# Kernel optimization log

Hardware: AMD Instinct MI355X
Metric: run time of the kernel (lower is better)

The kernel has to match this reference:

```python
import jax, jax.numpy as jnp
import numpy as np

B, NSV, NTRK, K, H = 512, 128, 512, 8, 16


def setup_inputs() -> dict:
    key = jax.random.key(0)
    ks = jax.random.split(key, 12)
    p = lambda k, shp: (jax.random.normal(k, shp, dtype=jnp.float32) * 0.1)
    return {
        "x_sv": jax.random.normal(ks[0], (B * NSV, 2), dtype=jnp.float32),
        "x_trk": jax.random.normal(ks[1], (B * NTRK, 8), dtype=jnp.float32),
        "batch_sv": jnp.repeat(jnp.arange(B, dtype=jnp.int32), NSV),
        "batch_trk": jnp.repeat(jnp.arange(B, dtype=jnp.int32), NTRK),
        # sv_encode: Linear(2,16) -> ELU -> Linear(16,16)
        "W1s": p(ks[2], (2, H)), "b1s": jnp.zeros((H,), jnp.float32),
        "W2s": p(ks[3], (H, H)), "b2s": jnp.zeros((H,), jnp.float32),
        # trk_encode: Linear(8,16) -> ELU -> Linear(16,16)
        "W1t": p(ks[4], (8, H)), "b1t": jnp.zeros((H,), jnp.float32),
        "W2t": p(ks[5], (H, H)), "b2t": jnp.zeros((H,), jnp.float32),
        # edge MLP: Linear(2*16, 16)
        "We": p(ks[6], (2 * H, H)), "be": jnp.zeros((H,), jnp.float32),
        # output head: Linear(16, 1)
        "Wo": p(ks[7], (H, 1)), "bo": jnp.zeros((1,), jnp.float32),
    }


def reference(x_sv, x_trk, batch_sv, batch_trk,
              W1s, b1s, W2s, b2s, W1t, b1t, W2t, b2t, We, be, Wo, bo):
    # Node encoders
    sv = jax.nn.elu(x_sv @ W1s + b1s) @ W2s + b2s      # [Nsv, H]
    trk = jax.nn.elu(x_trk @ W1t + b1t) @ W2t + b2t    # [Ntrk, H]

    # Regular batching: reshape to per-event blocks (batch_sv/batch_trk are
    # contiguous repeats of arange(B) with NSV / NTRK nodes per event).
    svb = sv.reshape(B, NSV, H)      # [B, S, H]
    trkb = trk.reshape(B, NTRK, H)   # [B, T, H]

    # kNN in encoded space: squared L2 distance per event, k nearest SVs per track
    t_sq = jnp.sum(trkb * trkb, -1)[:, :, None]          # [B, T, 1]
    s_sq = jnp.sum(svb * svb, -1)[:, None, :]            # [B, 1, S]
    dots = jnp.einsum("bth,bsh->bts", trkb, svb)         # [B, T, S]
    d2 = t_sq + s_sq - 2.0 * dots                        # [B, T, S]
    _, idx = jax.lax.top_k(-d2, K)                       # [B, T, K] indices into S

    # Gather neighbor SV features: [B, T, K, H]
    nbr = jax.vmap(lambda s, i: s[i])(svb, idx)

    # EdgeConv message: nn(cat[x_i, x_j - x_i]), x_i = track (target), x_j = SV
    ti = trkb[:, :, None, :]                                    # [B, T, 1, H]
    msg_in = jnp.concatenate(
        [jnp.broadcast_to(ti, nbr.shape), nbr - ti], axis=-1)   # [B, T, K, 2H]
    msg = msg_in @ We + be                                      # [B, T, K, H]
    feats = jnp.max(msg, axis=2).reshape(B * NTRK, H)           # max aggregation

    # Output head + per-event average pool (avg_pool_x with cluster == batch)
    out = jax.nn.sigmoid(feats @ Wo + bo)                       # [Ntrk, 1]
    sums = jax.ops.segment_sum(out, batch_trk, num_segments=B)  # [B, 1]
    cnts = jax.ops.segment_sum(jnp.ones_like(out), batch_trk, num_segments=B)
    pooled = sums / cnts                                        # [B, 1]
    batch_out = jnp.arange(B, dtype=jnp.int32)
    return pooled, batch_out
```

## Files before the change

### kernel.cpp

```cpp
#include <hip/hip_runtime.h>
#include <cmath>

#define BB   512
#define NSV  128
#define NTRK 512
#define KK   8
#define HH   16
#define TPB  512
#define PSTR 20

__device__ __forceinline__ float elu_f(float x) {
    return x > 0.0f ? x : expm1f(x);
}
__device__ __forceinline__ unsigned umin_u(unsigned a, unsigned b) { return a < b ? a : b; }
__device__ __forceinline__ unsigned umax_u(unsigned a, unsigned b) { return a > b ? a : b; }

__global__ __launch_bounds__(TPB, 4) void fused_net(
    const float* __restrict__ x_sv, const float* __restrict__ x_trk,
    const float* __restrict__ W1s, const float* __restrict__ b1s,
    const float* __restrict__ W2s, const float* __restrict__ b2s,
    const float* __restrict__ W1t, const float* __restrict__ b1t,
    const float* __restrict__ W2t, const float* __restrict__ b2t,
    const float* __restrict__ We,  const float* __restrict__ be,
    const float* __restrict__ Wo,  const float* __restrict__ bo,
    float* __restrict__ out)
{
    __shared__ float svf[NSV][HH];
    __shared__ float hsq[NSV];
    __shared__ float proj[NSV][PSTR];
    __shared__ float sWbot[HH][HH];
    __shared__ float sWdiff[HH][HH];
    __shared__ float sW1t[8][HH];
    __shared__ float sW2t[HH][HH];
    __shared__ float sb1t[HH], sb2t[HH], sbe[HH], sWo[HH];
    __shared__ float sred[TPB / 64];
    __shared__ float sbo;

    const int b   = blockIdx.x;
    const int tid = threadIdx.x;

    if (tid < HH * HH) {
        int j = tid >> 4, h = tid & 15;
        float top = We[j * HH + h];
        float bot = We[(HH + j) * HH + h];
        sWbot[j][h]  = bot;
        sWdiff[j][h] = top - bot;
        sW2t[j][h]   = W2t[tid];
    }
    if (tid < 8 * HH) sW1t[tid >> 4][tid & 15] = W1t[tid];
    if (tid < HH) {
        sb1t[tid] = b1t[tid];
        sb2t[tid] = b2t[tid];
        sbe[tid]  = be[tid];
        sWo[tid]  = Wo[tid];
    }
    if (tid == 0) sbo = bo[0];

    if (tid < NSV) {
        const float* xp = x_sv + (size_t)(b * NSV + tid) * 2;
        float x0 = xp[0], x1 = xp[1];
        float hbuf[HH];
        #pragma unroll
        for (int h = 0; h < HH; ++h)
            hbuf[h] = elu_f(x0 * W1s[h] + x1 * W1s[HH + h] + b1s[h]);
        float sq = 0.0f;
        #pragma unroll
        for (int h2 = 0; h2 < HH; ++h2) {
            float a = b2s[h2];
            #pragma unroll
            for (int h = 0; h < HH; ++h) a += hbuf[h] * W2s[h * HH + h2];
            svf[tid][h2] = a;
            sq += a * a;
        }
        hsq[tid] = 0.5f * sq;
    }
    __syncthreads();

    for (int e = tid; e < NSV * HH; e += TPB) {
        int s = e >> 4, h = e & 15;
        float a = 0.0f;
        #pragma unroll
        for (int j = 0; j < HH; ++j) a += svf[s][j] * sWbot[j][h];
        proj[s][h] = a;
    }

    const int t = tid;
    float tf[HH];
    float htsq;
    {
        const float* xp = x_trk + (size_t)(b * NTRK + t) * 8;
        float x[8];
        *(float4*)&x[0] = *(const float4*)&xp[0];
        *(float4*)&x[4] = *(const float4*)&xp[4];
        float hbuf[HH];
        #pragma unroll
        for (int h = 0; h < HH; ++h) {
            float a = sb1t[h];
            #pragma unroll
            for (int i = 0; i < 8; ++i) a += x[i] * sW1t[i][h];
            hbuf[h] = elu_f(a);
        }
        float sq = 0.0f;
        #pragma unroll
        for (int h2 = 0; h2 < HH; ++h2) {
            float a = sb2t[h2];
            #pragma unroll
            for (int h = 0; h < HH; ++h) a += hbuf[h] * sW2t[h][h2];
            tf[h2] = a;
            sq += a * a;
        }
        htsq = 0.5f * sq;
    }

    unsigned k[KK];
    #pragma unroll
    for (int q = 0; q < KK; ++q) k[q] = 0xFFFFFFFFu;
    __syncthreads();

    #pragma unroll 4
    for (int s = 0; s < NSV; ++s) {
        float4 s0 = *(const float4*)&svf[s][0];
        float4 s1 = *(const float4*)&svf[s][4];
        float4 s2 = *(const float4*)&svf[s][8];
        float4 s3 = *(const float4*)&svf[s][12];
        float hs = hsq[s];
        float a0 = fmaf(-tf[0], s0.x, htsq);
        float a1 = fmaf(-tf[1], s0.y, hs);
        float a2 = -tf[2] * s0.z;
        float a3 = -tf[3] * s0.w;
        a0 = fmaf(-tf[4],  s1.x, a0); a1 = fmaf(-tf[5],  s1.y, a1);
        a2 = fmaf(-tf[6],  s1.z, a2); a3 = fmaf(-tf[7],  s1.w, a3);
        a0 = fmaf(-tf[8],  s2.x, a0); a1 = fmaf(-tf[9],  s2.y, a1);
        a2 = fmaf(-tf[10], s2.z, a2); a3 = fmaf(-tf[11], s2.w, a3);
        a0 = fmaf(-tf[12], s3.x, a0); a1 = fmaf(-tf[13], s3.y, a1);
        a2 = fmaf(-tf[14], s3.z, a2); a3 = fmaf(-tf[15], s3.w, a3);
        float e = fmaxf((a0 + a1) + (a2 + a3), 0.0f);
        unsigned v = (__float_as_uint(e) & 0xFFFFFF80u) | (unsigned)s;
        #pragma unroll
        for (int q = 0; q < KK; ++q) {
            unsigned nk = umin_u(v, k[q]);
            v           = umax_u(v, k[q]);
            k[q] = nk;
        }
    }

    float local;
    {
        float base[HH];
        #pragma unroll
        for (int h = 0; h < HH; ++h) {
            float a = sbe[h];
            #pragma unroll
            for (int j = 0; j < HH; ++j) a += tf[j] * sWdiff[j][h];
            base[h] = a;
        }
        float mx[HH];
        #pragma unroll
        for (int h = 0; h < HH; ++h) mx[h] = -INFINITY;
        #pragma unroll
        for (int q = 0; q < KK; ++q) {
            const float* pr = &proj[k[q] & 127u][0];
            #pragma unroll
            for (int h4 = 0; h4 < 4; ++h4) {
                float4 p = *(const float4*)&pr[h4 * 4];
                mx[h4 * 4 + 0] = fmaxf(mx[h4 * 4 + 0], p.x);
                mx[h4 * 4 + 1] = fmaxf(mx[h4 * 4 + 1], p.y);
                mx[h4 * 4 + 2] = fmaxf(mx[h4 * 4 + 2], p.z);
                mx[h4 * 4 + 3] = fmaxf(mx[h4 * 4 + 3], p.w);
            }
        }
        float acc = sbo;
        #pragma unroll
        for (int h = 0; h < HH; ++h) acc += (base[h] + mx[h]) * sWo[h];
        local = 1.0f / (1.0f + expf(-acc));
    }

    #pragma unroll
    for (int off = 32; off > 0; off >>= 1)
        local += __shfl_down(local, off, 64);
    if ((tid & 63) == 0) sred[tid >> 6] = local;
    __syncthreads();
    if (tid == 0) {
        float tot = 0.0f;
        #pragma unroll
        for (int w = 0; w < TPB / 64; ++w) tot += sred[w];
        out[b]      = tot * (1.0f / NTRK);
        out[BB + b] = (float)b;
    }
}

extern "C" void kernel_launch(void* const* d_in, const int* in_sizes, int n_in,
                              void* d_out, int out_size, void* d_ws, size_t ws_size,
                              hipStream_t stream) {
    const float* x_sv  = (const float*)d_in[0];
    const float* x_trk = (const float*)d_in[1];
    const float* W1s = (const float*)d_in[4];
    const float* b1s = (const float*)d_in[5];
    const float* W2s = (const float*)d_in[6];
    const float* b2s = (const float*)d_in[7];
    const float* W1t = (const float*)d_in[8];
    const float* b1t = (const float*)d_in[9];
    const float* W2t = (const float*)d_in[10];
    const float* b2t = (const float*)d_in[11];
    const float* We  = (const float*)d_in[12];
    const float* be  = (const float*)d_in[13];
    const float* Wo  = (const float*)d_in[14];
    const float* bo  = (const float*)d_in[15];
    float* out = (float*)d_out;

    fused_net<<<BB, TPB, 0, stream>>>(x_sv, x_trk,
                                      W1s, b1s, W2s, b2s,
                                      W1t, b1t, W2t, b2t,
                                      We, be, Wo, bo, out);
}
```

Baseline: 136.6 us.

## Split SV encoding into precompute kernel and use med3 top-k insertion

Moves the SV encoder, projection, half-squared norms and weight difference into a separate precompute kernel that writes to workspace. The main kernel then reads SV features straight from global memory (uniform, scalar-cache friendly) instead of LDS, and keeps only proj in LDS. The sorted top-k insertion becomes a v_med3_u32 network, roughly halving the min/max ops per candidate, and weights and biases are read from global instead of staged in shared memory. This costs an extra launch and a global round trip for the SV data.

Result: slower. 139.4 us (+2.0%).

```diff
diff --git a/kernel.cpp b/kernel.cpp
--- a/kernel.cpp
+++ b/kernel.cpp
@@ -13,100 +13,111 @@
     return x > 0.0f ? x : expm1f(x);
 }
 __device__ __forceinline__ unsigned umin_u(unsigned a, unsigned b) { return a < b ? a : b; }
-__device__ __forceinline__ unsigned umax_u(unsigned a, unsigned b) { return a > b ? a : b; }
-
-__global__ __launch_bounds__(TPB, 4) void fused_net(
-    const float* __restrict__ x_sv, const float* __restrict__ x_trk,
+__device__ __forceinline__ unsigned med3u(unsigned a, unsigned b, unsigned c) {
+    unsigned d;
+    asm("v_med3_u32 %0, %1, %2, %3" : "=v"(d) : "v"(a), "v"(b), "v"(c));
+    return d;
+}
+
+__global__ __launch_bounds__(NSV) void precompute(
+    const float* __restrict__ x_sv,
     const float* __restrict__ W1s, const float* __restrict__ b1s,
     const float* __restrict__ W2s, const float* __restrict__ b2s,
+    const float* __restrict__ We,
+    float* __restrict__ svf_g, float* __restrict__ proj_g,
+    float* __restrict__ hsq_g, float* __restrict__ wdiff_g)
+{
+    const int b = blockIdx.x, s = threadIdx.x;
+
+    const float* xp = x_sv + (size_t)(b * NSV + s) * 2;
+    float x0 = xp[0], x1 = xp[1];
+    float hb[HH];
+    #pragma unroll
+    for (int h = 0; h < HH; ++h)
+        hb[h] = elu_f(x0 * W1s[h] + x1 * W1s[HH + h] + b1s[h]);
+
+    float o[HH];
+    float sq = 0.0f;
+    #pragma unroll
+    for (int h2 = 0; h2 < HH; ++h2) {
+        float a = b2s[h2];
+        #pragma unroll
+        for (int h = 0; h < HH; ++h) a += hb[h] * W2s[h * HH + h2];
+        o[h2] = a;
+        sq += a * a;
+    }
+
+    float* sdst = svf_g + (size_t)(b * NSV + s) * HH;
+    #pragma unroll
+    for (int h4 = 0; h4 < 4; ++h4)
+        *(float4*)&sdst[h4 * 4] = make_float4(o[h4*4], o[h4*4+1], o[h4*4+2], o[h4*4+3]);
+    hsq_g[b * NSV + s] = 0.5f * sq;
+
+    float* pdst = proj_g + (size_t)(b * NSV + s) * HH;
+    #pragma unroll
+    for (int h4 = 0; h4 < 4; ++h4) {
+        float p[4];
+        #pragma unroll
+        for (int q = 0; q < 4; ++q) {
+            int h = h4 * 4 + q;
+            float a = 0.0f;
+            #pragma unroll
+            for (int j = 0; j < HH; ++j) a += o[j] * We[(HH + j) * HH + h];
+            p[q] = a;
+        }
+        *(float4*)&pdst[h4 * 4] = make_float4(p[0], p[1], p[2], p[3]);
+    }
+
+    #pragma unroll
+    for (int r = 0; r < 2; ++r) {
+        int e = s * 2 + r;
+        wdiff_g[e] = We[e] - We[NSV * 2 + e];
+    }
+}
+
+__global__ __launch_bounds__(TPB, 4) void fused_main(
+    const float* __restrict__ x_trk,
     const float* __restrict__ W1t, const float* __restrict__ b1t,
     const float* __restrict__ W2t, const float* __restrict__ b2t,
-    const float* __restrict__ We,  const float* __restrict__ be,
-    const float* __restrict__ Wo,  const float* __restrict__ bo,
+    const float* __restrict__ be,  const float* __restrict__ Wo,
+    const float* __restrict__ bo,
+    const float* __restrict__ svf_g, const float* __restrict__ proj_g,
+    const float* __restrict__ hsq_g, const float* __restrict__ wdiff_g,
     float* __restrict__ out)
 {
-    __shared__ float svf[NSV][HH];
-    __shared__ float hsq[NSV];
     __shared__ float proj[NSV][PSTR];
-    __shared__ float sWbot[HH][HH];
-    __shared__ float sWdiff[HH][HH];
-    __shared__ float sW1t[8][HH];
-    __shared__ float sW2t[HH][HH];
-    __shared__ float sb1t[HH], sb2t[HH], sbe[HH], sWo[HH];
     __shared__ float sred[TPB / 64];
-    __shared__ float sbo;
-
-    const int b   = blockIdx.x;
-    const int tid = threadIdx.x;
-
-    if (tid < HH * HH) {
-        int j = tid >> 4, h = tid & 15;
-        float top = We[j * HH + h];
-        float bot = We[(HH + j) * HH + h];
-        sWbot[j][h]  = bot;
-        sWdiff[j][h] = top - bot;
-        sW2t[j][h]   = W2t[tid];
-    }
-    if (tid < 8 * HH) sW1t[tid >> 4][tid & 15] = W1t[tid];
-    if (tid < HH) {
-        sb1t[tid] = b1t[tid];
-        sb2t[tid] = b2t[tid];
-        sbe[tid]  = be[tid];
-        sWo[tid]  = Wo[tid];
-    }
-    if (tid == 0) sbo = bo[0];
-
-    if (tid < NSV) {
-        const float* xp = x_sv + (size_t)(b * NSV + tid) * 2;
-        float x0 = xp[0], x1 = xp[1];
-        float hbuf[HH];
-        #pragma unroll
-        for (int h = 0; h < HH; ++h)
-            hbuf[h] = elu_f(x0 * W1s[h] + x1 * W1s[HH + h] + b1s[h]);
-        float sq = 0.0f;
-        #pragma unroll
-        for (int h2 = 0; h2 < HH; ++h2) {
-            float a = b2s[h2];
-            #pragma unroll
-            for (int h = 0; h < HH; ++h) a += hbuf[h] * W2s[h * HH + h2];
-            svf[tid][h2] = a;
-            sq += a * a;
-        }
-        hsq[tid] = 0.5f * sq;
-    }
-    __syncthreads();
-
-    for (int e = tid; e < NSV * HH; e += TPB) {
-        int s = e >> 4, h = e & 15;
-        float a = 0.0f;
-        #pragma unroll
-        for (int j = 0; j < HH; ++j) a += svf[s][j] * sWbot[j][h];
-        proj[s][h] = a;
-    }
-
-    const int t = tid;
-    float tf[HH];
-    float htsq;
+
+    const int b = blockIdx.x, tid = threadIdx.x;
+
     {
-        const float* xp = x_trk + (size_t)(b * NTRK + t) * 8;
+        int s = tid >> 2, q = tid & 3;
+        float4 p = *(const float4*)&proj_g[(size_t)(b * NSV + s) * HH + q * 4];
+        *(float4*)&proj[s][q * 4] = p;
+    }
+
+    float tf[HH], ntf[HH], htsq;
+    {
+        const float* xp = x_trk + (size_t)(b * NTRK + tid) * 8;
         float x[8];
         *(float4*)&x[0] = *(const float4*)&xp[0];
         *(float4*)&x[4] = *(const float4*)&xp[4];
-        float hbuf[HH];
+        float hb[HH];
         #pragma unroll
         for (int h = 0; h < HH; ++h) {
-            float a = sb1t[h];
-            #pragma unroll
-            for (int i = 0; i < 8; ++i) a += x[i] * sW1t[i][h];
-            hbuf[h] = elu_f(a);
+            float a = b1t[h];
+            #pragma unroll
+            for (int i = 0; i < 8; ++i) a += x[i] * W1t[i * HH + h];
+            hb[h] = elu_f(a);
         }
         float sq = 0.0f;
         #pragma unroll
         for (int h2 = 0; h2 < HH; ++h2) {
-            float a = sb2t[h2];
-            #pragma unroll
-            for (int h = 0; h < HH; ++h) a += hbuf[h] * sW2t[h][h2];
+            float a = b2t[h2];
+            #pragma unroll
+            for (int h = 0; h < HH; ++h) a += hb[h] * W2t[h * HH + h2];
             tf[h2] = a;
+            ntf[h2] = -a;
             sq += a * a;
         }
         htsq = 0.5f * sq;
@@ -115,33 +126,38 @@
     unsigned k[KK];
     #pragma unroll
     for (int q = 0; q < KK; ++q) k[q] = 0xFFFFFFFFu;
+
     __syncthreads();
 
-    #pragma unroll 4
+    const float* __restrict__ svb = svf_g + (size_t)b * NSV * HH;
+    const float* __restrict__ hsb = hsq_g + (size_t)b * NSV;
+    #pragma unroll 2
     for (int s = 0; s < NSV; ++s) {
-        float4 s0 = *(const float4*)&svf[s][0];
-        float4 s1 = *(const float4*)&svf[s][4];
-        float4 s2 = *(const float4*)&svf[s][8];
-        float4 s3 = *(const float4*)&svf[s][12];
-        float hs = hsq[s];
-        float a0 = fmaf(-tf[0], s0.x, htsq);
-        float a1 = fmaf(-tf[1], s0.y, hs);
-        float a2 = -tf[2] * s0.z;
-        float a3 = -tf[3] * s0.w;
-        a0 = fmaf(-tf[4],  s1.x, a0); a1 = fmaf(-tf[5],  s1.y, a1);
-        a2 = fmaf(-tf[6],  s1.z, a2); a3 = fmaf(-tf[7],  s1.w, a3);
-        a0 = fmaf(-tf[8],  s2.x, a0); a1 = fmaf(-tf[9],  s2.y, a1);
-        a2 = fmaf(-tf[10], s2.z, a2); a3 = fmaf(-tf[11], s2.w, a3);
-        a0 = fmaf(-tf[12], s3.x, a0); a1 = fmaf(-tf[13], s3.y, a1);
-        a2 = fmaf(-tf[14], s3.z, a2); a3 = fmaf(-tf[15], s3.w, a3);
+        const float* sp = svb + s * HH;
+        float a0 = htsq, a1 = hsb[s];
+        a0 = fmaf(ntf[0], sp[0], a0);
+        a1 = fmaf(ntf[1], sp[1], a1);
+        float a2 = ntf[2] * sp[2];
+        float a3 = ntf[3] * sp[3];
+        #pragma unroll
+        for (int j = 4; j < HH; j += 4) {
+            a0 = fmaf(ntf[j],     sp[j],     a0);
+            a1 = fmaf(ntf[j + 1], sp[j + 1], a1);
+            a2 = fmaf(ntf[j + 2], sp[j + 2], a2);
+            a3 = fmaf(ntf[j + 3], sp[j + 3], a3);
+        }
         float e = fmaxf((a0 + a1) + (a2 + a3), 0.0f);
         unsigned v = (__float_as_uint(e) & 0xFFFFFF80u) | (unsigned)s;
-        #pragma unroll
-        for (int q = 0; q < KK; ++q) {
-            unsigned nk = umin_u(v, k[q]);
-            v           = umax_u(v, k[q]);
-            k[q] = nk;
-        }
+        unsigned nk0 = umin_u(v, k[0]);
+        unsigned nk1 = med3u(v, k[0], k[1]);
+        unsigned nk2 = med3u(v, k[1], k[2]);
+        unsigned nk3 = med3u(v, k[2], k[3]);
+        unsigned nk4 = med3u(v, k[3], k[4]);
+        unsigned nk5 = med3u(v, k[4], k[5]);
+        unsigned nk6 = med3u(v, k[5], k[6]);
+        unsigned nk7 = med3u(v, k[6], k[7]);
+        k[0] = nk0; k[1] = nk1; k[2] = nk2; k[3] = nk3;
+        k[4] = nk4; k[5] = nk5; k[6] = nk6; k[7] = nk7;
     }
 
     float local;
@@ -149,9 +165,9 @@
         float base[HH];
         #pragma unroll
         for (int h = 0; h < HH; ++h) {
-            float a = sbe[h];
-            #pragma unroll
-            for (int j = 0; j < HH; ++j) a += tf[j] * sWdiff[j][h];
+            float a = be[h];
+            #pragma unroll
+            for (int j = 0; j < HH; ++j) a += tf[j] * wdiff_g[j * HH + h];
             base[h] = a;
         }
         float mx[HH];
@@ -169,9 +185,9 @@
                 mx[h4 * 4 + 3] = fmaxf(mx[h4 * 4 + 3], p.w);
             }
         }
-        float acc = sbo;
-        #pragma unroll
-        for (int h = 0; h < HH; ++h) acc += (base[h] + mx[h]) * sWo[h];
+        float acc = bo[0];
+        #pragma unroll
+        for (int h = 0; h < HH; ++h) acc += (base[h] + mx[h]) * Wo[h];
         local = 1.0f / (1.0f + expf(-acc));
     }
 
@@ -208,8 +224,14 @@
     const float* bo  = (const float*)d_in[15];
     float* out = (float*)d_out;
 
-    fused_net<<<BB, TPB, 0, stream>>>(x_sv, x_trk,
-                                      W1s, b1s, W2s, b2s,
-                                      W1t, b1t, W2t, b2t,
-                                      We, be, Wo, bo, out);
-}
+    float* svf_g  = (float*)d_ws;
+    float* proj_g = svf_g  + (size_t)BB * NSV * HH;
+    float* hsq_g  = proj_g + (size_t)BB * NSV * HH;
+    float* wdiff_g = hsq_g + (size_t)BB * NSV;
+
+    precompute<<<BB, NSV, 0, stream>>>(x_sv, W1s, b1s, W2s, b2s, We,
+                                       svf_g, proj_g, hsq_g, wdiff_g);
+    fused_main<<<BB, TPB, 0, stream>>>(x_trk, W1t, b1t, W2t, b2t,
+                                       be, Wo, bo,
+                                       svf_g, proj_g, hsq_g, wdiff_g, out);
+}
```
